# Kernel tuning notes

Measured on AMD Instinct MI355X. Metric: run time of the kernel, lower is better.

Reference implementation:

```python
import jax, jax.numpy as jnp
import numpy as np


def setup_inputs() -> dict:
    key = jax.random.key(0)
    k1, k2, k3 = jax.random.split(key, 3)
    B, L, D = 4, 2056, 1024  # L = K + T = 8 + 2048
    x = jax.random.normal(k1, (B, L, D), dtype=jnp.float32)
    # Linear weights stored as (in_features, out_features); no bias (config.bias=False)
    W_attn = jax.random.normal(k2, (D, 3 * D), dtype=jnp.float32) * 0.02
    W_proj = jax.random.normal(k3, (D, D), dtype=jnp.float32) * 0.02
    return {"x": x, "W_attn": W_attn, "W_proj": W_proj, "n_head": 16, "n_memory": 8}


def reference(x, W_attn, W_proj, n_head, n_memory):
    B, L, C = x.shape
    K = n_memory
    T = L - K
    hd = C // n_head
    scale = 1.0 / np.sqrt(hd).astype(np.float32)

    qkv = x @ W_attn                      # (B, L, 3C)
    q, k, v = jnp.split(qkv, 3, axis=2)
    # (B, H, L, hd)
    q = q.reshape(B, L, n_head, hd).transpose(0, 2, 1, 3)
    k = k.reshape(B, L, n_head, hd).transpose(0, 2, 1, 3)
    v = v.reshape(B, L, n_head, hd).transpose(0, 2, 1, 3)

    att = jnp.einsum("bhqd,bhkd->bhqk", q, k) * scale  # (B, H, L, L)

    # Mask: all-True except the (seq x seq) block which is causal (lower-tri).
    # Memory rows (first K) attend everywhere; seq rows attend to all memory + causal seq.
    mask = jnp.ones((L, L), dtype=bool)
    seq_causal = jnp.tril(jnp.ones((T, T), dtype=bool))
    mask = mask.at[K:, K:].set(seq_causal)

    att = jnp.where(mask[None, None, :, :], att, jnp.float32(-jnp.inf))
    att = jax.nn.softmax(att, axis=-1)

    y = jnp.einsum("bhqk,bhkd->bhqd", att, v)  # (B, H, L, hd)
    y = y.transpose(0, 2, 1, 3).reshape(B, L, C)
    return y @ W_proj
```

## Files before the change

### kernel.cpp

```cpp
#include <hip/hip_runtime.h>
#include <hip/hip_bf16.h>
#include <hip/hip_fp16.h>

typedef _Float16 f16x8 __attribute__((ext_vector_type(8)));
typedef _Float16 f16x4 __attribute__((ext_vector_type(4)));
typedef float f32x4 __attribute__((ext_vector_type(4)));

typedef const __attribute__((address_space(1))) void gvoid_t;
typedef __attribute__((address_space(3))) void svoid_t;

constexpr int Bb = 4, Lq = 2056, Dd = 1024, NH = 16, HD = 64, NMEM = 8;
constexpr int Mtot = Bb * Lq;
constexpr int KEYS = 64;
constexpr int NT = (Lq + KEYS - 1) / KEYS;
constexpr int NTQP = 17;
constexpr int LqV = 2064;
constexpr int NCAST = (Mtot * Dd / 8) / 256;

__device__ inline float fexp2(float x) {
  float r;
  asm("v_exp_f32 %0, %1" : "=v"(r) : "v"(x));
  return r;
}

__global__ __launch_bounds__(256) void fused_prep(
    const float* __restrict__ x, const float* __restrict__ Wa,
    const float* __restrict__ Wp, _Float16* __restrict__ xh,
    _Float16* __restrict__ wta, _Float16* __restrict__ wtp) {
  const int gb = blockIdx.x;
  const int tid = threadIdx.x;
  if (gb < NCAST) {
    int i = gb * 256 + tid;
    const float4* p = reinterpret_cast<const float4*>(x) + (size_t)i * 2;
    float4 a = p[0], bq = p[1];
    f16x8 o;
    o[0] = (_Float16)a.x; o[1] = (_Float16)a.y; o[2] = (_Float16)a.z; o[3] = (_Float16)a.w;
    o[4] = (_Float16)bq.x; o[5] = (_Float16)bq.y; o[6] = (_Float16)bq.z; o[7] = (_Float16)bq.w;
    *(reinterpret_cast<f16x8*>(xh) + i) = o;
    return;
  }
  __shared__ float t[32][33];
  const float* in;
  _Float16* out;
  int rows = Dd, cols, bx, by;
  if (gb < NCAST + 3072) {
    int g = gb - NCAST;
    bx = g % 96; by = g / 96;
    in = Wa; out = wta; cols = 3 * Dd;
  } else {
    int g = gb - NCAST - 3072;
    bx = g & 31; by = g >> 5;
    in = Wp; out = wtp; cols = Dd;
  }
  const int tx = tid & 31, ty = tid >> 5;
  const int c0 = bx * 32, r0 = by * 32;
#pragma unroll
  for (int i = 0; i < 4; ++i)
    t[ty + i * 8][tx] = in[(size_t)(r0 + ty + i * 8) * cols + c0 + tx];
  __syncthreads();
#pragma unroll
  for (int i = 0; i < 4; ++i)
    out[(size_t)(c0 + ty + i * 8) * rows + r0 + tx] = (_Float16)t[tx][ty + i * 8];
}

template <int EPI>
__global__ __launch_bounds__(256) void gemm_f16(
    const _Float16* __restrict__ A, const _Float16* __restrict__ Bt,
    int M, int N, int Kd, float* __restrict__ Cf,
    _Float16* __restrict__ qout, _Float16* __restrict__ kout, _Float16* __restrict__ vtout) {
  constexpr int BM = 128, BN = 128, BK = 64;
  __shared__ _Float16 smem[2][2 * BM * BK];
  const int tid = threadIdx.x;
  const int wid = tid >> 6, lane = tid & 63;
  const int wr = wid >> 1, wc = wid & 1;
  const int l16 = lane & 15, lq = lane >> 4;

  const int gx = gridDim.x;
  const int nwg = gx * gridDim.y;
  const int i0 = blockIdx.y * gx + blockIdx.x;
  const int cpx = nwg >> 3;
  const int logical = (i0 & 7) * cpx + (i0 >> 3);
  const int m0 = (logical / gx) * BM, n0 = (logical % gx) * BN;

  f32x4 acc[4][4];
#pragma unroll
  for (int i = 0; i < 4; ++i)
#pragma unroll
    for (int j = 0; j < 4; ++j) acc[i][j] = (f32x4){0.f, 0.f, 0.f, 0.f};

  auto stage = [&](int sb, int kt) {
    const size_t kbase = (size_t)kt * BK;
    _Float16* sm = smem[sb];
#pragma unroll
    for (int c = 0; c < 4; ++c) {
      int q = wid * 256 + c * 64 + lane;
      int r = q >> 3, cc = q & 7;
      int gr = m0 + r; gr = gr < M ? gr : M - 1;
      const _Float16* src = A + (size_t)gr * Kd + kbase + ((cc ^ (r & 7)) << 3);
      __builtin_amdgcn_global_load_lds((gvoid_t*)src,
          (svoid_t*)(sm + (size_t)(wid * 256 + c * 64) * 8), 16, 0, 0);
    }
#pragma unroll
    for (int c = 0; c < 4; ++c) {
      int q = wid * 256 + c * 64 + lane;
      int r = q >> 3, cc = q & 7;
      const _Float16* src = Bt + (size_t)(n0 + r) * Kd + kbase + ((cc ^ (r & 7)) << 3);
      __builtin_amdgcn_global_load_lds((gvoid_t*)src,
          (svoid_t*)(sm + BM * BK + (size_t)(wid * 256 + c * 64) * 8), 16, 0, 0);
    }
  };

  const int KT = Kd / BK;
  stage(0, 0);
  __syncthreads();
  int sbuf = 0;
  for (int kt = 0; kt < KT; ++kt) {
    if (kt + 1 < KT) stage(sbuf ^ 1, kt + 1);
    const _Float16* sm = smem[sbuf];
#pragma unroll
    for (int kk = 0; kk < 2; ++kk) {
      f16x8 af[4], bfr[4];
#pragma unroll
      for (int i = 0; i < 4; ++i) {
        int r = wr * 64 + i * 16 + l16;
        int off = r * 64 + (((kk * 4 + lq) ^ (r & 7)) << 3);
        af[i] = *(const f16x8*)(sm + off);
      }
#pragma unroll
      for (int j = 0; j < 4; ++j) {
        int r = wc * 64 + j * 16 + l16;
        int off = BM * BK + r * 64 + (((kk * 4 + lq) ^ (r & 7)) << 3);
        bfr[j] = *(const f16x8*)(sm + off);
      }
#pragma unroll
      for (int i = 0; i < 4; ++i)
#pragma unroll
        for (int j = 0; j < 4; ++j)
          acc[i][j] = __builtin_amdgcn_mfma_f32_16x16x32_f16(af[i], bfr[j], acc[i][j], 0, 0, 0);
    }
    __syncthreads();
    sbuf ^= 1;
  }

  if (EPI == 1 && n0 >= 2 * Dd) {
#pragma unroll
    for (int i = 0; i < 4; ++i) {
      int mb = m0 + wr * 64 + i * 16 + lq * 4;
      if (mb >= M) continue;
      int b = mb / Lq, l = mb - b * Lq;
#pragma unroll
      for (int j = 0; j < 4; ++j) {
        int n = n0 + wc * 64 + j * 16 + l16;
        int h = (n >> 6) & 15, d = n & 63;
        if (l + 4 <= Lq) {
          int kk = l & 63;
          int ks = kk >> 5, rem = kk & 31, half = rem >> 4, idx = rem & 15;
          int col = (l & ~63) + (ks * 4 + (idx >> 2)) * 8 + half * 4;
          f16x4 pk;
          pk[0] = (_Float16)acc[i][j][0]; pk[1] = (_Float16)acc[i][j][1];
          pk[2] = (_Float16)acc[i][j][2]; pk[3] = (_Float16)acc[i][j][3];
          *(f16x4*)(vtout + ((size_t)(b * NH + h) * HD + d) * LqV + col) = pk;
        } else {
#pragma unroll
          for (int r = 0; r < 4; ++r) {
            int m = mb + r;
            if (m >= M) continue;
            int b2 = m / Lq, l2 = m - b2 * Lq;
            int kk = l2 & 63;
            int ks = kk >> 5, rem = kk & 31, half = rem >> 4, idx = rem & 15;
            int col = (l2 & ~63) + (ks * 4 + (idx >> 2)) * 8 + half * 4 + (idx & 3);
            vtout[((size_t)(b2 * NH + h) * HD + d) * LqV + col] = (_Float16)acc[i][j][r];
          }
        }
      }
    }
  } else {
#pragma unroll
    for (int i = 0; i < 4; ++i) {
#pragma unroll
      for (int r = 0; r < 4; ++r) {
        int m = m0 + wr * 64 + i * 16 + lq * 4 + r;
        if (m >= M) continue;
        if (EPI == 0) {
#pragma unroll
          for (int j = 0; j < 4; ++j) {
            int n = n0 + wc * 64 + j * 16 + l16;
            Cf[(size_t)m * N + n] = acc[i][j][r];
          }
        } else {
          int b = m / Lq, l = m - b * Lq;
#pragma unroll
          for (int j = 0; j < 4; ++j) {
            int n = n0 + wc * 64 + j * 16 + l16;
            int which = n >> 10, h = (n >> 6) & 15, d = n & 63;
            int bh = b * NH + h;
            _Float16 v = (_Float16)acc[i][j][r];
            if (which == 0)
              qout[((size_t)bh * Lq + l) * HD + d] = v;
            else
              kout[((size_t)bh * Lq + l) * HD + d] = v;
          }
        }
      }
    }
  }
}

__global__ __launch_bounds__(256) void attn_f16(const _Float16* __restrict__ qm,
                                                const _Float16* __restrict__ km,
                                                const _Float16* __restrict__ vt,
                                                _Float16* __restrict__ y) {
  __shared__ _Float16 kls[2][KEYS * HD];
  __shared__ _Float16 vls[2][KEYS * HD];

  const int i0 = blockIdx.y * (int)gridDim.x + blockIdx.x;
  const int logical = (i0 & 7) * (NTQP * Bb * NH / 8) + (i0 >> 3);
  const int bh = logical / NTQP;
  const int px = logical % NTQP;

  const int wid = threadIdx.x >> 6, lane = threadIdx.x & 63;
  const int l16 = lane & 15, lq = lane >> 4;

  const _Float16* qbase = qm + (size_t)bh * Lq * HD;
  const _Float16* kbase = km + (size_t)bh * Lq * HD;
  const _Float16* vbase = vt + (size_t)bh * HD * LqV;
  const int b = bh >> 4, h = bh & 15;

  const _Float16 QSC = (_Float16)(0.125f * 1.44269504f);

  f16x8 ones;
#pragma unroll
  for (int e = 0; e < 8; ++e) ones[e] = (_Float16)1.0f;

  const int qA = (wid * 2 + 0) * 64 + lane, qB = (wid * 2 + 1) * 64 + lane;
  const int rA = qA >> 3, cA = qA & 7;
  const int rB = qB >> 3, cB = qB & 7;
  const int ofA = (cA ^ (rA & 7)) << 3;
  const int ofB = (cB ^ (rB & 7)) << 3;
  _Float16* dKA0 = &kls[0][(wid * 2 + 0) * 512]; _Float16* dKB0 = &kls[0][(wid * 2 + 1) * 512];
  _Float16* dKA1 = &kls[1][(wid * 2 + 0) * 512]; _Float16* dKB1 = &kls[1][(wid * 2 + 1) * 512];
  _Float16* dVA0 = &vls[0][(wid * 2 + 0) * 512]; _Float16* dVB0 = &vls[0][(wid * 2 + 1) * 512];
  _Float16* dVA1 = &vls[1][(wid * 2 + 0) * 512]; _Float16* dVB1 = &vls[1][(wid * 2 + 1) * 512];

  const int nseg = (px == 0) ? 1 : 2;
  for (int seg = 0; seg < nseg; ++seg) {
    const int qt = (px == 0) ? 0 : (seg == 0 ? NT - px : px);
    const int qr0 = qt * 64 + wid * 16;

    int qrow = qr0 + l16; if (qrow > Lq - 1) qrow = Lq - 1;
    f16x8 qf0 = *(const f16x8*)(qbase + (size_t)qrow * HD + lq * 8);
    f16x8 qf1 = *(const f16x8*)(qbase + (size_t)qrow * HD + 32 + lq * 8);
#pragma unroll
    for (int e = 0; e < 8; ++e) {
      qf0[e] *= QSC;
      qf1[e] *= QSC;
    }

    const int irow = qr0 + l16;
    const int kmax = (irow < NMEM) ? (Lq - 1) : (irow < Lq - 1 ? irow : Lq - 1);

    f32x4 o[4];
#pragma unroll
    for (int dt = 0; dt < 4; ++dt) o[dt] = (f32x4){0.f, 0.f, 0.f, 0.f};
    f32x4 ol = (f32x4){0.f, 0.f, 0.f, 0.f};

    const int ntiles = (qt == 0) ? NT : (qt + 1 < NT ? qt + 1 : NT);

    const _Float16* pkA = kbase + (size_t)rA * HD + ofA;
    const _Float16* pkB = kbase + (size_t)rB * HD + ofB;
    const _Float16* pvA = vbase + (size_t)rA * LqV + ofA;
    const _Float16* pvB = vbase + (size_t)rB * LqV + ofB;

    auto stage_fast = [&](_Float16* dK0, _Float16* dK1, _Float16* dV0, _Float16* dV1) {
      __builtin_amdgcn_global_load_lds((gvoid_t*)pkA, (svoid_t*)dK0, 16, 0, 0);
      __builtin_amdgcn_global_load_lds((gvoid_t*)pkB, (svoid_t*)dK1, 16, 0, 0);
      __builtin_amdgcn_global_load_lds((gvoid_t*)pvA, (svoid_t*)dV0, 16, 0, 0);
      __builtin_amdgcn_global_load_lds((gvoid_t*)pvB, (svoid_t*)dV1, 16, 0, 0);
      pkA += KEYS * HD; pkB += KEYS * HD; pvA += KEYS; pvB += KEYS;
    };
    auto stage_clamp = [&](_Float16* dK0, _Float16* dK1, _Float16* dV0, _Float16* dV1) {
      int keyA = 2048 + rA; if (keyA > Lq - 1) keyA = Lq - 1;
      int keyB = 2048 + rB; if (keyB > Lq - 1) keyB = Lq - 1;
      __builtin_amdgcn_global_load_lds((gvoid_t*)(kbase + (size_t)keyA * HD + ofA),
                                       (svoid_t*)dK0, 16, 0, 0);
      __builtin_amdgcn_global_load_lds((gvoid_t*)(kbase + (size_t)keyB * HD + ofB),
                                       (svoid_t*)dK1, 16, 0, 0);
      int kcA = 2048 + ofA; if (kcA + 8 > LqV) kcA = LqV - 8;
      int kcB = 2048 + ofB; if (kcB + 8 > LqV) kcB = LqV - 8;
      __builtin_amdgcn_global_load_lds((gvoid_t*)(vbase + (size_t)rA * LqV + kcA),
                                       (svoid_t*)dV0, 16, 0, 0);
      __builtin_amdgcn_global_load_lds((gvoid_t*)(vbase + (size_t)rB * LqV + kcB),
                                       (svoid_t*)dV1, 16, 0, 0);
    };

    auto compute = [&](const _Float16* Kl, const _Float16* Vl, int t) {
      const bool fastw = ((t + 1) * KEYS <= qr0);
      const int lim = kmax - t * KEYS;
#pragma unroll
      for (int ks = 0; ks < 2; ++ks) {
        const int r0 = ks * 32 + l16, r1 = r0 + 16;
        f16x8 ka0 = *(const f16x8*)(Kl + r0 * 64 + ((lq ^ (r0 & 7)) << 3));
        f16x8 kb0 = *(const f16x8*)(Kl + r0 * 64 + (((4 + lq) ^ (r0 & 7)) << 3));
        f16x8 ka1 = *(const f16x8*)(Kl + r1 * 64 + ((lq ^ (r1 & 7)) << 3));
        f16x8 kb1 = *(const f16x8*)(Kl + r1 * 64 + (((4 + lq) ^ (r1 & 7)) << 3));
        f32x4 s0 = (f32x4){0.f, 0.f, 0.f, 0.f};
        f32x4 s1 = (f32x4){0.f, 0.f, 0.f, 0.f};
        __builtin_amdgcn_s_setprio(1);
        s0 = __builtin_amdgcn_mfma_f32_16x16x32_f16(ka0, qf0, s0, 0, 0, 0);
        s0 = __builtin_amdgcn_mfma_f32_16x16x32_f16(kb0, qf1, s0, 0, 0, 0);
        s1 = __builtin_amdgcn_mfma_f32_16x16x32_f16(ka1, qf0, s1, 0, 0, 0);
        s1 = __builtin_amdgcn_mfma_f32_16x16x32_f16(kb1, qf1, s1, 0, 0, 0);
        __builtin_amdgcn_s_setprio(0);

        f16x8 pf;
        if (fastw) {
#pragma unroll
          for (int r = 0; r < 4; ++r) {
            pf[r] = (_Float16)fexp2(s0[r]);
            pf[4 + r] = (_Float16)fexp2(s1[r]);
          }
        } else {
          const int kb = ks * 32 + lq * 4;
#pragma unroll
          for (int r = 0; r < 4; ++r) {
            pf[r] = (kb + r <= lim) ? (_Float16)fexp2(s0[r]) : (_Float16)0.f;
            pf[4 + r] = (kb + 16 + r <= lim) ? (_Float16)fexp2(s1[r]) : (_Float16)0.f;
          }
        }

        __builtin_amdgcn_s_setprio(1);
        ol = __builtin_amdgcn_mfma_f32_16x16x32_f16(pf, ones, ol, 0, 0, 0);
#pragma unroll
        for (int dt = 0; dt < 4; ++dt) {
          const int vr = dt * 16 + l16;
          const int g = ks * 4 + lq;
          f16x8 vf = *(const f16x8*)(Vl + vr * 64 + ((g ^ (vr & 7)) << 3));
          o[dt] = __builtin_amdgcn_mfma_f32_16x16x32_f16(pf, vf, o[dt], 0, 0, 0);
        }
        __builtin_amdgcn_s_setprio(0);
      }
    };

    stage_fast(dKA0, dKB0, dVA0, dVB0);
    __syncthreads();
    int t = 0;
    for (;;) {
      {
        int nxt = t + 1;
        if (nxt < ntiles) {
          if (nxt == NT - 1) stage_clamp(dKA1, dKB1, dVA1, dVB1);
          else stage_fast(dKA1, dKB1, dVA1, dVB1);
        }
      }
      compute(kls[0], vls[0], t);
      __syncthreads();
      if (++t >= ntiles) break;
      {
        int nxt = t + 1;
        if (nxt < ntiles) {
          if (nxt == NT - 1) stage_clamp(dKA0, dKB0, dVA0, dVB0);
          else stage_fast(dKA0, dKB0, dVA0, dVB0);
        }
      }
      compute(kls[1], vls[1], t);
      __syncthreads();
      if (++t >= ntiles) break;
    }

#pragma unroll
    for (int r = 0; r < 4; ++r) {
      int orow = qr0 + lq * 4 + r;
      if (orow >= Lq) continue;
      float inv = 1.0f / ol[r];
#pragma unroll
      for (int dt = 0; dt < 4; ++dt)
        y[((size_t)(b * Lq + orow)) * Dd + h * HD + dt * 16 + l16] = (_Float16)(o[dt][r] * inv);
    }
  }
}

extern "C" void kernel_launch(void* const* d_in, const int* in_sizes, int n_in,
                              void* d_out, int out_size, void* d_ws, size_t ws_size,
                              hipStream_t stream) {
  (void)in_sizes; (void)n_in; (void)out_size; (void)ws_size;
  const float* x = (const float*)d_in[0];
  const float* W_attn = (const float*)d_in[1];
  const float* W_proj = (const float*)d_in[2];
  float* out = (float*)d_out;

  char* w = (char*)d_ws;
  _Float16* xh  = (_Float16*)(w);
  _Float16* wta = (_Float16*)(w + 16842752);
  _Float16* wtp = (_Float16*)(w + 23134208);
  _Float16* qh  = (_Float16*)(w + 25231360);
  _Float16* kh  = (_Float16*)(w + 42074112);
  _Float16* vth = (_Float16*)(w + 58916864);
  _Float16* yh  = xh;

  fused_prep<<<dim3(NCAST + 3072 + 1024), dim3(256), 0, stream>>>(
      x, W_attn, W_proj, xh, wta, wtp);

  gemm_f16<1><<<dim3(3 * Dd / 128, (Mtot + 127) / 128), dim3(256), 0, stream>>>(
      xh, wta, Mtot, 3 * Dd, Dd, nullptr, qh, kh, vth);

  attn_f16<<<dim3(NTQP, Bb * NH), dim3(256), 0, stream>>>(qh, kh, vth, yh);

  gemm_f16<0><<<dim3(Dd / 128, (Mtot + 127) / 128), dim3(256), 0, stream>>>(
      yh, wtp, Mtot, Dd, Dd, out, nullptr, nullptr, nullptr);
}
```

Baseline: 200.4 us.

## Enlarge attention query tile to 128 rows with two 16-row groups per wave

Each attention block now handles one 128-row query tile, and each wave computes two 16-row query groups against every staged K/V tile. This replaces the earlier scheme of 64-row tiles processed as paired causal segments. Every K/V tile loaded into LDS is reused by twice as many queries, which halves global-to-LDS staging and barrier count per query. In exchange, accumulator registers double, which may lower occupancy. Load balance now depends on ordering blocks heavy-first rather than on pairing short and long causal rows.

```diff
diff --git a/kernel.cpp b/kernel.cpp
--- a/kernel.cpp
+++ b/kernel.cpp
@@ -13,7 +13,7 @@
 constexpr int Mtot = Bb * Lq;
 constexpr int KEYS = 64;
 constexpr int NT = (Lq + KEYS - 1) / KEYS;
-constexpr int NTQP = 17;
+constexpr int QTILES = 17;
 constexpr int LqV = 2064;
 constexpr int NCAST = (Mtot * Dd / 8) / 256;
 
@@ -214,12 +214,14 @@
   __shared__ _Float16 vls[2][KEYS * HD];
 
   const int i0 = blockIdx.y * (int)gridDim.x + blockIdx.x;
-  const int logical = (i0 & 7) * (NTQP * Bb * NH / 8) + (i0 >> 3);
-  const int bh = logical / NTQP;
-  const int px = logical % NTQP;
+  const int logical = (i0 & 7) * (QTILES * Bb * NH / 8) + (i0 >> 3);
+  const int bh = logical / QTILES;
+  const int qtl = logical % QTILES;
+  const int qt = (qtl == 0) ? 16 : ((qtl == 1) ? 0 : QTILES - qtl);
 
   const int wid = threadIdx.x >> 6, lane = threadIdx.x & 63;
   const int l16 = lane & 15, lq = lane >> 4;
+  const int qr0 = qt * 128 + wid * 32;
 
   const _Float16* qbase = qm + (size_t)bh * Lq * HD;
   const _Float16* kbase = km + (size_t)bh * Lq * HD;
@@ -231,6 +233,35 @@
   f16x8 ones;
 #pragma unroll
   for (int e = 0; e < 8; ++e) ones[e] = (_Float16)1.0f;
+
+  int qrow0 = qr0 + l16;      if (qrow0 > Lq - 1) qrow0 = Lq - 1;
+  int qrow1 = qr0 + 16 + l16; if (qrow1 > Lq - 1) qrow1 = Lq - 1;
+  f16x8 qfa0 = *(const f16x8*)(qbase + (size_t)qrow0 * HD + lq * 8);
+  f16x8 qfa1 = *(const f16x8*)(qbase + (size_t)qrow0 * HD + 32 + lq * 8);
+  f16x8 qfb0 = *(const f16x8*)(qbase + (size_t)qrow1 * HD + lq * 8);
+  f16x8 qfb1 = *(const f16x8*)(qbase + (size_t)qrow1 * HD + 32 + lq * 8);
+#pragma unroll
+  for (int e = 0; e < 8; ++e) {
+    qfa0[e] *= QSC; qfa1[e] *= QSC;
+    qfb0[e] *= QSC; qfb1[e] *= QSC;
+  }
+
+  const int irow0 = qr0 + l16;
+  const int irow1 = qr0 + 16 + l16;
+  const int kmax0 = (irow0 < NMEM) ? (Lq - 1) : (irow0 < Lq - 1 ? irow0 : Lq - 1);
+  const int kmax1 = (irow1 < NMEM) ? (Lq - 1) : (irow1 < Lq - 1 ? irow1 : Lq - 1);
+
+  f32x4 o0[4], o1[4];
+#pragma unroll
+  for (int dt = 0; dt < 4; ++dt) {
+    o0[dt] = (f32x4){0.f, 0.f, 0.f, 0.f};
+    o1[dt] = (f32x4){0.f, 0.f, 0.f, 0.f};
+  }
+  f32x4 ol0 = (f32x4){0.f, 0.f, 0.f, 0.f};
+  f32x4 ol1 = (f32x4){0.f, 0.f, 0.f, 0.f};
+
+  const int nt2 = 2 * qt + 2;
+  const int ntiles = (qt == 0) ? NT : (nt2 < NT ? nt2 : NT);
 
   const int qA = (wid * 2 + 0) * 64 + lane, qB = (wid * 2 + 1) * 64 + lane;
   const int rA = qA >> 3, cA = qA & 7;
@@ -242,139 +273,147 @@
   _Float16* dVA0 = &vls[0][(wid * 2 + 0) * 512]; _Float16* dVB0 = &vls[0][(wid * 2 + 1) * 512];
   _Float16* dVA1 = &vls[1][(wid * 2 + 0) * 512]; _Float16* dVB1 = &vls[1][(wid * 2 + 1) * 512];
 
-  const int nseg = (px == 0) ? 1 : 2;
-  for (int seg = 0; seg < nseg; ++seg) {
-    const int qt = (px == 0) ? 0 : (seg == 0 ? NT - px : px);
-    const int qr0 = qt * 64 + wid * 16;
-
-    int qrow = qr0 + l16; if (qrow > Lq - 1) qrow = Lq - 1;
-    f16x8 qf0 = *(const f16x8*)(qbase + (size_t)qrow * HD + lq * 8);
-    f16x8 qf1 = *(const f16x8*)(qbase + (size_t)qrow * HD + 32 + lq * 8);
-#pragma unroll
-    for (int e = 0; e < 8; ++e) {
-      qf0[e] *= QSC;
-      qf1[e] *= QSC;
-    }
-
-    const int irow = qr0 + l16;
-    const int kmax = (irow < NMEM) ? (Lq - 1) : (irow < Lq - 1 ? irow : Lq - 1);
-
-    f32x4 o[4];
-#pragma unroll
-    for (int dt = 0; dt < 4; ++dt) o[dt] = (f32x4){0.f, 0.f, 0.f, 0.f};
-    f32x4 ol = (f32x4){0.f, 0.f, 0.f, 0.f};
-
-    const int ntiles = (qt == 0) ? NT : (qt + 1 < NT ? qt + 1 : NT);
-
-    const _Float16* pkA = kbase + (size_t)rA * HD + ofA;
-    const _Float16* pkB = kbase + (size_t)rB * HD + ofB;
-    const _Float16* pvA = vbase + (size_t)rA * LqV + ofA;
-    const _Float16* pvB = vbase + (size_t)rB * LqV + ofB;
-
-    auto stage_fast = [&](_Float16* dK0, _Float16* dK1, _Float16* dV0, _Float16* dV1) {
-      __builtin_amdgcn_global_load_lds((gvoid_t*)pkA, (svoid_t*)dK0, 16, 0, 0);
-      __builtin_amdgcn_global_load_lds((gvoid_t*)pkB, (svoid_t*)dK1, 16, 0, 0);
-      __builtin_amdgcn_global_load_lds((gvoid_t*)pvA, (svoid_t*)dV0, 16, 0, 0);
-      __builtin_amdgcn_global_load_lds((gvoid_t*)pvB, (svoid_t*)dV1, 16, 0, 0);
-      pkA += KEYS * HD; pkB += KEYS * HD; pvA += KEYS; pvB += KEYS;
-    };
-    auto stage_clamp = [&](_Float16* dK0, _Float16* dK1, _Float16* dV0, _Float16* dV1) {
-      int keyA = 2048 + rA; if (keyA > Lq - 1) keyA = Lq - 1;
-      int keyB = 2048 + rB; if (keyB > Lq - 1) keyB = Lq - 1;
-      __builtin_amdgcn_global_load_lds((gvoid_t*)(kbase + (size_t)keyA * HD + ofA),
-                                       (svoid_t*)dK0, 16, 0, 0);
-      __builtin_amdgcn_global_load_lds((gvoid_t*)(kbase + (size_t)keyB * HD + ofB),
-                                       (svoid_t*)dK1, 16, 0, 0);
-      int kcA = 2048 + ofA; if (kcA + 8 > LqV) kcA = LqV - 8;
-      int kcB = 2048 + ofB; if (kcB + 8 > LqV) kcB = LqV - 8;
-      __builtin_amdgcn_global_load_lds((gvoid_t*)(vbase + (size_t)rA * LqV + kcA),
-                                       (svoid_t*)dV0, 16, 0, 0);
-      __builtin_amdgcn_global_load_lds((gvoid_t*)(vbase + (size_t)rB * LqV + kcB),
-                                       (svoid_t*)dV1, 16, 0, 0);
-    };
-
-    auto compute = [&](const _Float16* Kl, const _Float16* Vl, int t) {
-      const bool fastw = ((t + 1) * KEYS <= qr0);
-      const int lim = kmax - t * KEYS;
-#pragma unroll
-      for (int ks = 0; ks < 2; ++ks) {
-        const int r0 = ks * 32 + l16, r1 = r0 + 16;
-        f16x8 ka0 = *(const f16x8*)(Kl + r0 * 64 + ((lq ^ (r0 & 7)) << 3));
-        f16x8 kb0 = *(const f16x8*)(Kl + r0 * 64 + (((4 + lq) ^ (r0 & 7)) << 3));
-        f16x8 ka1 = *(const f16x8*)(Kl + r1 * 64 + ((lq ^ (r1 & 7)) << 3));
-        f16x8 kb1 = *(const f16x8*)(Kl + r1 * 64 + (((4 + lq) ^ (r1 & 7)) << 3));
-        f32x4 s0 = (f32x4){0.f, 0.f, 0.f, 0.f};
-        f32x4 s1 = (f32x4){0.f, 0.f, 0.f, 0.f};
-        __builtin_amdgcn_s_setprio(1);
-        s0 = __builtin_amdgcn_mfma_f32_16x16x32_f16(ka0, qf0, s0, 0, 0, 0);
-        s0 = __builtin_amdgcn_mfma_f32_16x16x32_f16(kb0, qf1, s0, 0, 0, 0);
-        s1 = __builtin_amdgcn_mfma_f32_16x16x32_f16(ka1, qf0, s1, 0, 0, 0);
-        s1 = __builtin_amdgcn_mfma_f32_16x16x32_f16(kb1, qf1, s1, 0, 0, 0);
-        __builtin_amdgcn_s_setprio(0);
-
-        f16x8 pf;
-        if (fastw) {
-#pragma unroll
-          for (int r = 0; r < 4; ++r) {
-            pf[r] = (_Float16)fexp2(s0[r]);
-            pf[4 + r] = (_Float16)fexp2(s1[r]);
-          }
-        } else {
-          const int kb = ks * 32 + lq * 4;
-#pragma unroll
-          for (int r = 0; r < 4; ++r) {
-            pf[r] = (kb + r <= lim) ? (_Float16)fexp2(s0[r]) : (_Float16)0.f;
-            pf[4 + r] = (kb + 16 + r <= lim) ? (_Float16)fexp2(s1[r]) : (_Float16)0.f;
-          }
-        }
-
-        __builtin_amdgcn_s_setprio(1);
-        ol = __builtin_amdgcn_mfma_f32_16x16x32_f16(pf, ones, ol, 0, 0, 0);
-#pragma unroll
-        for (int dt = 0; dt < 4; ++dt) {
-          const int vr = dt * 16 + l16;
-          const int g = ks * 4 + lq;
-          f16x8 vf = *(const f16x8*)(Vl + vr * 64 + ((g ^ (vr & 7)) << 3));
-          o[dt] = __builtin_amdgcn_mfma_f32_16x16x32_f16(pf, vf, o[dt], 0, 0, 0);
-        }
-        __builtin_amdgcn_s_setprio(0);
-      }
-    };
-
-    stage_fast(dKA0, dKB0, dVA0, dVB0);
+  const _Float16* pkA = kbase + (size_t)rA * HD + ofA;
+  const _Float16* pkB = kbase + (size_t)rB * HD + ofB;
+  const _Float16* pvA = vbase + (size_t)rA * LqV + ofA;
+  const _Float16* pvB = vbase + (size_t)rB * LqV + ofB;
+
+  auto stage_fast = [&](_Float16* dK0, _Float16* dK1, _Float16* dV0, _Float16* dV1) {
+    __builtin_amdgcn_global_load_lds((gvoid_t*)pkA, (svoid_t*)dK0, 16, 0, 0);
+    __builtin_amdgcn_global_load_lds((gvoid_t*)pkB, (svoid_t*)dK1, 16, 0, 0);
+    __builtin_amdgcn_global_load_lds((gvoid_t*)pvA, (svoid_t*)dV0, 16, 0, 0);
+    __builtin_amdgcn_global_load_lds((gvoid_t*)pvB, (svoid_t*)dV1, 16, 0, 0);
+    pkA += KEYS * HD; pkB += KEYS * HD; pvA += KEYS; pvB += KEYS;
+  };
+  auto stage_clamp = [&](_Float16* dK0, _Float16* dK1, _Float16* dV0, _Float16* dV1) {
+    int keyA = 2048 + rA; if (keyA > Lq - 1) keyA = Lq - 1;
+    int keyB = 2048 + rB; if (keyB > Lq - 1) keyB = Lq - 1;
+    __builtin_amdgcn_global_load_lds((gvoid_t*)(kbase + (size_t)keyA * HD + ofA),
+                                     (svoid_t*)dK0, 16, 0, 0);
+    __builtin_amdgcn_global_load_lds((gvoid_t*)(kbase + (size_t)keyB * HD + ofB),
+                                     (svoid_t*)dK1, 16, 0, 0);
+    int kcA = 2048 + ofA; if (kcA + 8 > LqV) kcA = LqV - 8;
+    int kcB = 2048 + ofB; if (kcB + 8 > LqV) kcB = LqV - 8;
+    __builtin_amdgcn_global_load_lds((gvoid_t*)(vbase + (size_t)rA * LqV + kcA),
+                                     (svoid_t*)dV0, 16, 0, 0);
+    __builtin_amdgcn_global_load_lds((gvoid_t*)(vbase + (size_t)rB * LqV + kcB),
+                                     (svoid_t*)dV1, 16, 0, 0);
+  };
+
+  auto compute = [&](const _Float16* Kl, const _Float16* Vl, int t) {
+    const bool fast0 = ((t + 1) * KEYS <= qr0);
+    const bool fast1 = ((t + 1) * KEYS <= qr0 + 16);
+    const int lim0 = kmax0 - t * KEYS;
+    const int lim1 = kmax1 - t * KEYS;
+#pragma unroll
+    for (int ks = 0; ks < 2; ++ks) {
+      const int r0 = ks * 32 + l16, r1 = r0 + 16;
+      f16x8 ka0 = *(const f16x8*)(Kl + r0 * 64 + ((lq ^ (r0 & 7)) << 3));
+      f16x8 kb0 = *(const f16x8*)(Kl + r0 * 64 + (((4 + lq) ^ (r0 & 7)) << 3));
+      f16x8 ka1 = *(const f16x8*)(Kl + r1 * 64 + ((lq ^ (r1 & 7)) << 3));
+      f16x8 kb1 = *(const f16x8*)(Kl + r1 * 64 + (((4 + lq) ^ (r1 & 7)) << 3));
+      f32x4 sa0 = (f32x4){0.f, 0.f, 0.f, 0.f};
+      f32x4 sa1 = (f32x4){0.f, 0.f, 0.f, 0.f};
+      f32x4 sb0 = (f32x4){0.f, 0.f, 0.f, 0.f};
+      f32x4 sb1 = (f32x4){0.f, 0.f, 0.f, 0.f};
+      __builtin_amdgcn_s_setprio(1);
+      sa0 = __builtin_amdgcn_mfma_f32_16x16x32_f16(ka0, qfa0, sa0, 0, 0, 0);
+      sa0 = __builtin_amdgcn_mfma_f32_16x16x32_f16(kb0, qfa1, sa0, 0, 0, 0);
+      sa1 = __builtin_amdgcn_mfma_f32_16x16x32_f16(ka1, qfa0, sa1, 0, 0, 0);
+      sa1 = __builtin_amdgcn_mfma_f32_16x16x32_f16(kb1, qfa1, sa1, 0, 0, 0);
+      sb0 = __builtin_amdgcn_mfma_f32_16x16x32_f16(ka0, qfb0, sb0, 0, 0, 0);
+      sb0 = __builtin_amdgcn_mfma_f32_16x16x32_f16(kb0, qfb1, sb0, 0, 0, 0);
+      sb1 = __builtin_amdgcn_mfma_f32_16x16x32_f16(ka1, qfb0, sb1, 0, 0, 0);
+      sb1 = __builtin_amdgcn_mfma_f32_16x16x32_f16(kb1, qfb1, sb1, 0, 0, 0);
+      __builtin_amdgcn_s_setprio(0);
+
+      const int kb = ks * 32 + lq * 4;
+      f16x8 pf0, pf1;
+      if (fast0) {
+#pragma unroll
+        for (int r = 0; r < 4; ++r) {
+          pf0[r] = (_Float16)fexp2(sa0[r]);
+          pf0[4 + r] = (_Float16)fexp2(sa1[r]);
+        }
+      } else {
+#pragma unroll
+        for (int r = 0; r < 4; ++r) {
+          pf0[r] = (kb + r <= lim0) ? (_Float16)fexp2(sa0[r]) : (_Float16)0.f;
+          pf0[4 + r] = (kb + 16 + r <= lim0) ? (_Float16)fexp2(sa1[r]) : (_Float16)0.f;
+        }
+      }
+      if (fast1) {
+#pragma unroll
+        for (int r = 0; r < 4; ++r) {
+          pf1[r] = (_Float16)fexp2(sb0[r]);
+          pf1[4 + r] = (_Float16)fexp2(sb1[r]);
+        }
+      } else {
+#pragma unroll
+        for (int r = 0; r < 4; ++r) {
+          pf1[r] = (kb + r <= lim1) ? (_Float16)fexp2(sb0[r]) : (_Float16)0.f;
+          pf1[4 + r] = (kb + 16 + r <= lim1) ? (_Float16)fexp2(sb1[r]) : (_Float16)0.f;
+        }
+      }
+
+      __builtin_amdgcn_s_setprio(1);
+      ol0 = __builtin_amdgcn_mfma_f32_16x16x32_f16(pf0, ones, ol0, 0, 0, 0);
+      ol1 = __builtin_amdgcn_mfma_f32_16x16x32_f16(pf1, ones, ol1, 0, 0, 0);
+#pragma unroll
+      for (int dt = 0; dt < 4; ++dt) {
+        const int vr = dt * 16 + l16;
+        const int g = ks * 4 + lq;
+        f16x8 vf = *(const f16x8*)(Vl + vr * 64 + ((g ^ (vr & 7)) << 3));
+        o0[dt] = __builtin_amdgcn_mfma_f32_16x16x32_f16(pf0, vf, o0[dt], 0, 0, 0);
+        o1[dt] = __builtin_amdgcn_mfma_f32_16x16x32_f16(pf1, vf, o1[dt], 0, 0, 0);
+      }
+      __builtin_amdgcn_s_setprio(0);
+    }
+  };
+
+  stage_fast(dKA0, dKB0, dVA0, dVB0);
+  __syncthreads();
+  int t = 0;
+  for (;;) {
+    {
+      int nxt = t + 1;
+      if (nxt < ntiles) {
+        if (nxt == NT - 1) stage_clamp(dKA1, dKB1, dVA1, dVB1);
+        else stage_fast(dKA1, dKB1, dVA1, dVB1);
+      }
+    }
+    compute(kls[0], vls[0], t);
     __syncthreads();
-    int t = 0;
-    for (;;) {
-      {
-        int nxt = t + 1;
-        if (nxt < ntiles) {
-          if (nxt == NT - 1) stage_clamp(dKA1, dKB1, dVA1, dVB1);
-          else stage_fast(dKA1, dKB1, dVA1, dVB1);
-        }
-      }
-      compute(kls[0], vls[0], t);
-      __syncthreads();
-      if (++t >= ntiles) break;
-      {
-        int nxt = t + 1;
-        if (nxt < ntiles) {
-          if (nxt == NT - 1) stage_clamp(dKA0, dKB0, dVA0, dVB0);
-          else stage_fast(dKA0, dKB0, dVA0, dVB0);
-        }
-      }
-      compute(kls[1], vls[1], t);
-      __syncthreads();
-      if (++t >= ntiles) break;
-    }
-
-#pragma unroll
-    for (int r = 0; r < 4; ++r) {
-      int orow = qr0 + lq * 4 + r;
-      if (orow >= Lq) continue;
-      float inv = 1.0f / ol[r];
+    if (++t >= ntiles) break;
+    {
+      int nxt = t + 1;
+      if (nxt < ntiles) {
+        if (nxt == NT - 1) stage_clamp(dKA0, dKB0, dVA0, dVB0);
+        else stage_fast(dKA0, dKB0, dVA0, dVB0);
+      }
+    }
+    compute(kls[1], vls[1], t);
+    __syncthreads();
+    if (++t >= ntiles) break;
+  }
+
+#pragma unroll
+  for (int r = 0; r < 4; ++r) {
+    int orow = qr0 + lq * 4 + r;
+    if (orow < Lq) {
+      float inv = 1.0f / ol0[r];
 #pragma unroll
       for (int dt = 0; dt < 4; ++dt)
-        y[((size_t)(b * Lq + orow)) * Dd + h * HD + dt * 16 + l16] = (_Float16)(o[dt][r] * inv);
+        y[((size_t)(b * Lq + orow)) * Dd + h * HD + dt * 16 + l16] =
+            (_Float16)(o0[dt][r] * inv);
+    }
+    int orow1 = qr0 + 16 + lq * 4 + r;
+    if (orow1 < Lq) {
+      float inv = 1.0f / ol1[r];
+#pragma unroll
+      for (int dt = 0; dt < 4; ++dt)
+        y[((size_t)(b * Lq + orow1)) * Dd + h * HD + dt * 16 + l16] =
+            (_Float16)(o1[dt][r] * inv);
     }
   }
 }
@@ -403,7 +442,7 @@
   gemm_f16<1><<<dim3(3 * Dd / 128, (Mtot + 127) / 128), dim3(256), 0, stream>>>(
       xh, wta, Mtot, 3 * Dd, Dd, nullptr, qh, kh, vth);
 
-  attn_f16<<<dim3(NTQP, Bb * NH), dim3(256), 0, stream>>>(qh, kh, vth, yh);
+  attn_f16<<<dim3(QTILES, Bb * NH), dim3(256), 0, stream>>>(qh, kh, vth, yh);
 
   gemm_f16<0><<<dim3(Dd / 128, (Mtot + 127) / 128), dim3(256), 0, stream>>>(
       yh, wtp, Mtot, Dd, Dd, out, nullptr, nullptr, nullptr);
```

Result: slower. 224.7 us (+12.1%).
